# Kernel tuning notes

Hardware: AMD Instinct MI355X
Metric: run time of the kernel (lower is better)

## Reference

```python
import jax, jax.numpy as jnp
import numpy as np
from jax import lax

B, C, H, W = 8, 128, 64, 64
L = H * W  # 4096, multiple of 64 so BiMamba2's pad-to-chunk is a no-op
DM, DI, DS, DC, NH, HD = 32, 64, 64, 4, 1, 64  # d_model, d_inner, d_state, d_conv, nheads, headdim


def setup_inputs() -> dict:
    key = jax.random.key(0)
    ks = jax.random.split(key, 12)
    def r(i, shape, s):
        return jax.random.normal(ks[i], shape, jnp.float32) * s
    return {
        "x": jax.random.normal(ks[0], (B, C, H, W), jnp.float32),
        "lin1_w": r(1, (C, C), 0.05), "lin1_b": jnp.zeros((C,), jnp.float32),
        "dw_w": r(2, (C, 1, 3, 3), 0.1), "dw_b": jnp.zeros((C,), jnp.float32),
        "fc_in_w": r(3, (C, DM), 0.05),
        "mam_in_w": r(4, (2, DM, 2 * DI + 2 * DS + NH), 0.05),
        "mam_conv_w": r(5, (2, DI + 2 * DS, DC), 0.1),
        "mam_conv_b": jnp.zeros((2, DI + 2 * DS), jnp.float32),
        "mam_dt_bias": r(6, (2, NH), 0.1),
        "mam_A_log": jnp.zeros((2, NH), jnp.float32),
        "mam_D": jnp.ones((2, NH), jnp.float32),
        "mam_norm_w": jnp.ones((2, DI), jnp.float32),
        "mam_out_w": r(7, (2, DI, DM), 0.05),
        "fc_out_w": r(8, (DM, C), 0.05),
        "bn_g": jnp.ones((C,), jnp.float32), "bn_b": jnp.zeros((C,), jnp.float32),
        "conv4_w": r(9, (C, C), 0.05), "conv4_b": jnp.zeros((C,), jnp.float32),
    }


def _causal_dwconv1d(x, w, b):
    # x: (B, L, Ch); w: (Ch, DC) depthwise causal kernel (torch Conv1d groups=Ch, pad=DC-1, trimmed)
    xc = jnp.transpose(x, (0, 2, 1))
    xc = jnp.pad(xc, ((0, 0), (0, 0), (DC - 1, 0)))
    o = lax.conv_general_dilated(xc, w[:, None, :], (1,), "VALID",
                                 feature_group_count=w.shape[0],
                                 dimension_numbers=("NCH", "OIH", "NCH"))
    return jnp.transpose(o + b[None, :, None], (0, 2, 1))


def _mamba2(u, W_in, conv_w, conv_b, dt_bias, A_log, D, norm_w, W_out):
    # u: (B, L, DM). Minimal Mamba2 block: in_proj -> causal dwconv/silu -> selective scan -> gated RMSNorm -> out_proj
    b, l, _ = u.shape
    zxbcdt = u @ W_in                         # (b, l, 2*DI + 2*DS + NH)
    z = zxbcdt[..., :DI]
    xBC = zxbcdt[..., DI:DI + DI + 2 * DS]
    dt = zxbcdt[..., -NH:]
    xBC = jax.nn.silu(_causal_dwconv1d(xBC, conv_w, conv_b))
    xs = xBC[..., :DI]
    Bm = xBC[..., DI:DI + DS]                 # (b, l, DS)
    Cm = xBC[..., DI + DS:]                   # (b, l, DS)
    dt = jax.nn.softplus(dt + dt_bias)        # (b, l, NH)
    dA = jnp.exp(dt * (-jnp.exp(A_log)))      # (b, l, NH)
    xh = xs.reshape(b, l, NH, HD)
    dtx = dt[..., None] * xh                  # (b, l, NH, HD)

    def step(h, inp):
        dA_t, dtx_t, B_t, C_t = inp
        h = dA_t[:, :, None, None] * h + dtx_t[..., None] * B_t[:, None, None, :]
        y = jnp.einsum("bhpn,bn->bhp", h, C_t)
        return h, y

    h0 = jnp.zeros((b, NH, HD, DS), u.dtype)
    _, ys = lax.scan(step, h0, (jnp.moveaxis(dA, 1, 0), jnp.moveaxis(dtx, 1, 0),
                                jnp.moveaxis(Bm, 1, 0), jnp.moveaxis(Cm, 1, 0)))
    y = jnp.moveaxis(ys, 0, 1) + D[None, None, :, None] * xh   # (b, l, NH, HD)
    y = y.reshape(b, l, DI)
    y = y * jax.nn.silu(z)                    # gated RMSNorm
    y = y * lax.rsqrt(jnp.mean(y * y, -1, keepdims=True) + 1e-5) * norm_w
    return y @ W_out                          # (b, l, DM)


def _forward(x, lin1_w, lin1_b, dw_w, dw_b, fc_in_w, mam_in_w, mam_conv_w, mam_conv_b,
             mam_dt_bias, mam_A_log, mam_D, mam_norm_w, mam_out_w, fc_out_w,
             bn_g, bn_b, conv4_w, conv4_b):
    b, c, h, w = x.shape
    o = jnp.einsum("bihw,io->bohw", x, lin1_w) + lin1_b[None, :, None, None]
    o = lax.conv_general_dilated(o, dw_w, (1, 1), "SAME", feature_group_count=c,
                                 dimension_numbers=("NCHW", "OIHW", "NCHW")) + dw_b[None, :, None, None]
    o = jax.nn.silu(o)
    # BiMamba2_2D: flatten HxW -> sequence, fc_in, forward + reversed Mamba2, fc_out
    s = jnp.einsum("bcl,cd->bld", o.reshape(b, c, h * w), fc_in_w)
    y1 = _mamba2(s, mam_in_w[0], mam_conv_w[0], mam_conv_b[0], mam_dt_bias[0],
                 mam_A_log[0], mam_D[0], mam_norm_w[0], mam_out_w[0])
    y2 = jnp.flip(_mamba2(jnp.flip(s, 1), mam_in_w[1], mam_conv_w[1], mam_conv_b[1],
                          mam_dt_bias[1], mam_A_log[1], mam_D[1], mam_norm_w[1], mam_out_w[1]), 1)
    o = jnp.transpose((y1 + y2) @ fc_out_w, (0, 2, 1)).reshape(b, c, h, w)
    # BatchNorm2d (training-mode batch statistics)
    mu = jnp.mean(o, (0, 2, 3), keepdims=True)
    var = jnp.mean((o - mu) ** 2, (0, 2, 3), keepdims=True)
    o = (o - mu) * lax.rsqrt(var + 1e-5) * bn_g[None, :, None, None] + bn_b[None, :, None, None]
    g = jax.nn.sigmoid(jnp.einsum("bihw,io->bohw", o, conv4_w) + conv4_b[None, :, None, None])
    return g * x + x


def reference(x, lin1_w, lin1_b, dw_w, dw_b, fc_in_w, mam_in_w, mam_conv_w, mam_conv_b,
              mam_dt_bias, mam_A_log, mam_D, mam_norm_w, mam_out_w, fc_out_w,
              bn_g, bn_b, conv4_w, conv4_b):
    return _forward(x, lin1_w, lin1_b, dw_w, dw_b, fc_in_w, mam_in_w, mam_conv_w, mam_conv_b,
                    mam_dt_bias, mam_A_log, mam_D, mam_norm_w, mam_out_w, fc_out_w,
                    bn_g, bn_b, conv4_w, conv4_b)
```

## Files before the change

kernel.cpp:

```cpp
#include <hip/hip_runtime.h>
#include <math.h>

constexpr int Bn = 8, Cn = 128, Ln = 4096;

constexpr size_t OFF_O1   = 0;
constexpr size_t OFF_O2   = 4194304;
constexpr size_t OFF_S    = 8388608;
constexpr size_t OFF_Z    = 9437184;
constexpr size_t OFF_WT   = 11534336;
constexpr size_t OFF_XBCA = 13631488;
constexpr size_t OFF_DTS  = 26214400;
constexpr size_t OFF_CUM  = 26279936;
constexpr size_t OFF_T    = 26345472;
constexpr size_t OFF_SPREV= 30539776;
constexpr size_t OFF_S2A  = 34734080;
constexpr size_t OFF_S2B  = 35782656;
constexpr size_t OFF_BN   = 36831232;
constexpr size_t OFF_XX   = 36831488;
constexpr size_t OFF_WB1  = 38928640;
constexpr size_t OFF_WB4  = 38936832;
constexpr size_t OFF_WN   = 38945024;
constexpr size_t OFF_O3   = 0;

constexpr long XSTRIDE_H = 6291456;
constexpr long TSTRIDE = 2097152;

typedef __attribute__((ext_vector_type(8))) short short8;
typedef __attribute__((ext_vector_type(4))) float f32x4;
typedef __attribute__((ext_vector_type(4))) unsigned short us4;
typedef __attribute__((ext_vector_type(8))) unsigned short us8;

__device__ __forceinline__ float siluf(float v) { return v / (1.0f + expf(-v)); }

__device__ __forceinline__ unsigned short tobf(float f) {
  unsigned int u = __float_as_uint(f);
  u += 0x7FFFu + ((u >> 16) & 1u);
  return (unsigned short)(u >> 16);
}

__device__ __forceinline__ float frombf(unsigned short u) {
  return __uint_as_float(((unsigned int)u) << 16);
}

__device__ __forceinline__ unsigned int pk2(float a, float b) {
  return (unsigned int)tobf(a) | ((unsigned int)tobf(b) << 16);
}

__device__ __forceinline__ short8 ldfrag(const unsigned short* p) {
  union { unsigned int u[4]; short8 s; } cv;
  cv.u[0] = *(const unsigned int*)(p);
  cv.u[1] = *(const unsigned int*)(p + 2);
  cv.u[2] = *(const unsigned int*)(p + 4);
  cv.u[3] = *(const unsigned int*)(p + 6);
  return cv.s;
}

__global__ void k_prepc(const float* __restrict__ lin1_w, const float* __restrict__ conv4_w,
                        const float* __restrict__ normw, const float* __restrict__ Wout,
                        unsigned short* __restrict__ wb1, unsigned short* __restrict__ wb4,
                        unsigned short* __restrict__ wn) {
  int blk = blockIdx.x, tid = threadIdx.x;
  if (blk < 2) {
    const float* src = blk ? conv4_w : lin1_w;
    unsigned short* dst = blk ? wb4 : wb1;
    for (int idx = tid * 4; idx < 16384; idx += 1024) {
      float4 v = *(const float4*)&src[idx];
      us4 o;
      o[0] = tobf(v.x); o[1] = tobf(v.y); o[2] = tobf(v.z); o[3] = tobf(v.w);
      *(us4*)&dst[idx] = o;
    }
  } else {
    int dir = blk - 2;
    for (int idx = tid; idx < 2048; idx += 256) {
      int d = idx >> 6, p = idx & 63;
      wn[dir * 2048 + idx] = tobf(normw[dir * 64 + p] * Wout[(long)dir * 2048 + p * 32 + d]);
    }
  }
}

__global__ __launch_bounds__(256) void k_lin1(const float* __restrict__ x,
                                              const unsigned short* __restrict__ wb,
                                              const float* __restrict__ bias,
                                              unsigned short* __restrict__ o1) {
  __shared__ unsigned short wT[64][140];
  __shared__ unsigned short xT[64][140];
  int b = blockIdx.y, l0 = blockIdx.x * 64, cb = blockIdx.z * 64;
  int tid = threadIdx.x, lane = tid & 63, mt = tid >> 6;
  int q = lane >> 4, i = lane & 15;
  int c4 = (tid & 15) * 4, k0 = (tid >> 4) * 2;
#pragma unroll
  for (int s = 0; s < 4; ++s) {
    int k = k0 + s * 32;
    us4 w0 = *(const us4*)&wb[k * 128 + cb + c4];
    us4 w1 = *(const us4*)&wb[(k + 1) * 128 + cb + c4];
#pragma unroll
    for (int j = 0; j < 4; ++j)
      *(unsigned int*)&wT[c4 + j][k] =
          (unsigned int)w0[j] | ((unsigned int)w1[j] << 16);
    float4 x0 = *(const float4*)&x[((long)b * 128 + k) * 4096 + l0 + c4];
    float4 x1 = *(const float4*)&x[((long)b * 128 + k + 1) * 4096 + l0 + c4];
    *(unsigned int*)&xT[c4 + 0][k] = pk2(x0.x, x1.x);
    *(unsigned int*)&xT[c4 + 1][k] = pk2(x0.y, x1.y);
    *(unsigned int*)&xT[c4 + 2][k] = pk2(x0.z, x1.z);
    *(unsigned int*)&xT[c4 + 3][k] = pk2(x0.w, x1.w);
  }
  __syncthreads();
  short8 af[4];
#pragma unroll
  for (int kk = 0; kk < 4; ++kk)
    af[kk] = ldfrag(&wT[mt * 16 + i][q * 8 + 32 * kk]);
  float bv[4];
#pragma unroll
  for (int r2 = 0; r2 < 4; ++r2) bv[r2] = bias[cb + 16 * mt + q * 4 + r2];
#pragma unroll
  for (int nt = 0; nt < 4; ++nt) {
    f32x4 d = {0.f, 0.f, 0.f, 0.f};
#pragma unroll
    for (int kk = 0; kk < 4; ++kk) {
      short8 bfr = ldfrag(&xT[nt * 16 + i][q * 8 + 32 * kk]);
      d = __builtin_amdgcn_mfma_f32_16x16x32_bf16(af[kk], bfr, d, 0, 0, 0);
    }
#pragma unroll
    for (int r2 = 0; r2 < 4; ++r2) {
      int c = 16 * mt + q * 4 + r2;
      o1[((long)b * 128 + cb + c) * 4096 + l0 + nt * 16 + i] = tobf(d[r2] + bv[r2]);
    }
  }
}

__global__ void k_dw(const unsigned short* __restrict__ o1,
                     const float* __restrict__ wgt,
                     const float* __restrict__ bias, unsigned short* __restrict__ o2) {
  __shared__ float p[4096];
  int bc = blockIdx.x, c = bc & 127, tid = threadIdx.x;
  const unsigned short* src = o1 + (long)bc * 4096;
#pragma unroll
  for (int s4 = 0; s4 < 2; ++s4) {
    int off = s4 * 2048 + tid * 8;
    us8 v = *(const us8*)&src[off];
#pragma unroll
    for (int j = 0; j < 8; ++j) p[off + j] = frombf(v[j]);
  }
  float wr[9];
#pragma unroll
  for (int j = 0; j < 9; ++j) wr[j] = wgt[c * 9 + j];
  float bv = bias[c];
  __syncthreads();
  int wg = tid & 15, hs = tid >> 4;
  int w0 = wg * 4, h0 = hs * 4;
  float in[6][6];
#pragma unroll
  for (int ri = 0; ri < 6; ++ri) {
    int h = h0 - 1 + ri;
    if (h < 0 || h > 63) {
#pragma unroll
      for (int ci = 0; ci < 6; ++ci) in[ri][ci] = 0.f;
    } else {
      float4 cc = *(float4*)&p[h * 64 + w0];
      in[ri][1] = cc.x; in[ri][2] = cc.y; in[ri][3] = cc.z; in[ri][4] = cc.w;
      in[ri][0] = (w0 > 0) ? p[h * 64 + w0 - 1] : 0.f;
      in[ri][5] = (w0 < 60) ? p[h * 64 + w0 + 4] : 0.f;
    }
  }
#pragma unroll
  for (int r = 0; r < 4; ++r) {
    us4 oc;
#pragma unroll
    for (int q = 0; q < 4; ++q) {
      float acc = bv;
#pragma unroll
      for (int dh = 0; dh < 3; ++dh)
#pragma unroll
        for (int dq = 0; dq < 3; ++dq)
          acc += in[r + dh][q + dq] * wr[dh * 3 + dq];
      oc[q] = tobf(siluf(acc));
    }
    *(us4*)&o2[(long)bc * 4096 + (h0 + r) * 64 + w0] = oc;
  }
}

__global__ void k_fcin(const unsigned short* __restrict__ o2, const float* __restrict__ w,
                       unsigned short* __restrict__ sb,
                       const float* __restrict__ Win, unsigned short* __restrict__ WT) {
  __shared__ float xt[128][64];
  __shared__ float wt[128][32];
  int b = blockIdx.y, l0 = blockIdx.x * 64;
  int tid = threadIdx.x;
  int f4 = (tid & 15) * 4, r0 = tid >> 4;
#pragma unroll
  for (int st = 0; st < 8; ++st) {
    int r = r0 + st * 16;
    us4 v = *(const us4*)&o2[((long)b * 128 + r) * 4096 + l0 + f4];
#pragma unroll
    for (int j = 0; j < 4; ++j) xt[r][f4 + j] = frombf(v[j]);
  }
  int f4w = (tid & 7) * 4, rw = tid >> 3;
#pragma unroll
  for (int st = 0; st < 4; ++st) {
    int r = rw + st * 32;
    *(float4*)&wt[r][f4w] = *(const float4*)&w[r * 32 + f4w];
  }
  __syncthreads();
  int tx = tid & 15, ty = tid >> 4;
  int c0 = tx * 4, d0 = ty * 2;
  float acc[2][4] = {};
  for (int k = 0; k < 128; ++k) {
    float4 xv = *(float4*)&xt[k][c0];
    float2 wv = *(float2*)&wt[k][d0];
    float xa[4] = {xv.x, xv.y, xv.z, xv.w};
#pragma unroll
    for (int q = 0; q < 4; ++q) {
      acc[0][q] += wv.x * xa[q];
      acc[1][q] += wv.y * xa[q];
    }
  }
#pragma unroll
  for (int q = 0; q < 4; ++q) {
    long ob = ((long)b * 4096 + l0 + c0 + q) * 32 + d0;
    *(unsigned int*)&sb[ob] = pk2(acc[0][q], acc[1][q]);
  }
  if (blockIdx.y == 0 && blockIdx.x < 2) {
    int dir = blockIdx.x;
    for (int idx = tid; idx < 272 * 32; idx += 256) {
      int n = idx >> 5, kk = idx & 31;
      float v = (n < 257) ? Win[dir * 32 * 257 + kk * 257 + n] : 0.f;
      WT[dir * 8704 + idx] = tobf(v);
    }
  }
}

__global__ __launch_bounds__(256) void k_inprojconv(
    const unsigned short* __restrict__ sb, const unsigned short* __restrict__ WT,
    const float* __restrict__ conv_w, const float* __restrict__ conv_b,
    const float* __restrict__ dt_bias, const float* __restrict__ A_log,
    unsigned short* __restrict__ zT, unsigned short* __restrict__ xbca,
    unsigned short* __restrict__ xX,
    float* __restrict__ dts, float* __restrict__ cum,
    unsigned short* __restrict__ Tg) {
  __shared__ unsigned short xbcT[192][82];
  __shared__ float dtL[64];
  __shared__ float dtsS[64], cumSS[64], fL[64];
  int dir = blockIdx.z, b = blockIdx.y, l0 = blockIdx.x * 64;
  int tid = threadIdx.x, lane = tid & 63, mt = tid >> 6;
  int q = lane >> 4, i = lane & 15;
  long rowbase = (long)b * 4096 + l0;
  const unsigned short* W = WT + (long)dir * 8704;
  const short8 zfrag = {0, 0, 0, 0, 0, 0, 0, 0};

  if (mt == 0) {
    short8 afr[4];
#pragma unroll
    for (int rt = 0; rt < 4; ++rt) {
      int l = l0 + 16 * rt + i;
      int lsrc = dir ? (4095 - l) : l;
      afr[rt] = *(const short8*)&sb[((long)b * 4096 + lsrc) * 32 + q * 8];
    }
#pragma unroll
    for (int ct = 0; ct < 4; ++ct) {
      int n = 16 * ct + i;
      short8 bfr = *(const short8*)&W[n * 32 + q * 8];
      unsigned short* zrow = zT + (((long)dir * 64 + n) * 8 + b) * 4096 + l0 + q * 4;
#pragma unroll
      for (int rt = 0; rt < 4; ++rt) {
        f32x4 d = {0.f, 0.f, 0.f, 0.f};
        d = __builtin_amdgcn_mfma_f32_16x16x32_bf16(afr[rt], bfr, d, 0, 0, 0);
        us4 pk;
        pk[0] = tobf(d[0]); pk[1] = tobf(d[1]);
        pk[2] = tobf(d[2]); pk[3] = tobf(d[3]);
        *(us4*)&zrow[16 * rt] = pk;
      }
    }
    {
      short8 bfr = *(const short8*)&W[(256 + i) * 32 + q * 8];
#pragma unroll
      for (int rt = 0; rt < 4; ++rt) {
        f32x4 d = {0.f, 0.f, 0.f, 0.f};
        d = __builtin_amdgcn_mfma_f32_16x16x32_bf16(afr[rt], bfr, d, 0, 0, 0);
        if (i == 0) {
#pragma unroll
          for (int r2 = 0; r2 < 4; ++r2) dtL[16 * rt + q * 4 + r2] = d[r2];
        }
      }
    }
  } else {
    short8 afr[5];
#pragma unroll
    for (int rt = 0; rt < 5; ++rt) {
      int l = l0 - 3 + 16 * rt + i;
      if (l >= 0 && l < 4096) {
        int lsrc = dir ? (4095 - l) : l;
        afr[rt] = *(const short8*)&sb[((long)b * 4096 + lsrc) * 32 + q * 8];
      } else {
        afr[rt] = zfrag;
      }
    }
#pragma unroll
    for (int cti = 0; cti < 4; ++cti) {
      int n = 16 * (mt * 4 + cti) + i;
      short8 bfr = *(const short8*)&W[n * 32 + q * 8];
      int cc = n - 64;
#pragma unroll
      for (int rt = 0; rt < 5; ++rt) {
        f32x4 d = {0.f, 0.f, 0.f, 0.f};
        d = __builtin_amdgcn_mfma_f32_16x16x32_bf16(afr[rt], bfr, d, 0, 0, 0);
        int rr0 = 16 * rt + q * 4;
        unsigned int p0 = (unsigned int)tobf(d[0]) | ((unsigned int)tobf(d[1]) << 16);
        unsigned int p1 = (unsigned int)tobf(d[2]) | ((unsigned int)tobf(d[3]) << 16);
        *(unsigned int*)&xbcT[cc][rr0] = p0;
        *(unsigned int*)&xbcT[cc][rr0 + 2] = p1;
      }
    }
  }
  __syncthreads();

  if (tid < 192) {
    int c = tid;
    float cw0 = conv_w[dir * 768 + c * 4 + 0];
    float cw1 = conv_w[dir * 768 + c * 4 + 1];
    float cw2 = conv_w[dir * 768 + c * 4 + 2];
    float cw3 = conv_w[dir * 768 + c * 4 + 3];
    float cb2 = conv_b[dir * 192 + c];
    unsigned short* xp = xbca + (long)dir * XSTRIDE_H;
    float win0 = 0.f, win1 = 0.f, win2 = 0.f, win3 = 0.f;
    for (int rp = 0; rp < 34; ++rp) {
      unsigned int pk = *(const unsigned int*)&xbcT[c][rp * 2];
      float a0 = frombf((unsigned short)(pk & 0xFFFFu));
      float a1 = frombf((unsigned short)(pk >> 16));
      int rr = rp * 2;
      win0 = win1; win1 = win2; win2 = win3; win3 = a0;
      if (rr >= 3 && rr <= 66) {
        float acc = cb2 + win0 * cw0 + win1 * cw1 + win2 * cw2 + win3 * cw3;
        float sv = siluf(acc);
        int t = rr - 3;
        if (c >= 64) xp[(rowbase + t) * 192 + c] = tobf(sv);
        if (c < 128) xbcT[c][t] = tobf(sv);
      }
      win0 = win1; win1 = win2; win2 = win3; win3 = a1;
      if (rr + 1 >= 3 && rr + 1 <= 66) {
        float acc = cb2 + win0 * cw0 + win1 * cw1 + win2 * cw2 + win3 * cw3;
        float sv = siluf(acc);
        int t = rr - 2;
        if (c >= 64) xp[(rowbase + t) * 192 + c] = tobf(sv);
        if (c < 128) xbcT[c][t] = tobf(sv);
      }
    }
  } else {
    int ln = tid - 192;
    float v = dtL[ln] + dt_bias[dir];
    float sp = (v > 20.f) ? v : log1pf(expf(v));
    dts[dir * 32768 + rowbase + ln] = sp;
    dtsS[ln] = sp;
    float cd = -expf(A_log[dir]) * sp;
#pragma unroll
    for (int off = 1; off < 64; off <<= 1) {
      float u = __shfl_up(cd, off);
      if (ln >= off) cd += u;
    }
    cum[dir * 32768 + rowbase + ln] = cd;
    cumSS[ln] = cd;
  }
  __syncthreads();

  {
    int r = tid >> 2, seg = (tid & 3) * 16;
    unsigned short* dst =
        xX + (((long)dir * 512 + b * 64 + blockIdx.x) * 64 + r) * 64 + seg;
#pragma unroll
    for (int j = 0; j < 8; ++j) {
      unsigned int v = *(const unsigned int*)&xbcT[r][seg + 2 * j];
      *(unsigned int*)(dst + 2 * j) = v;
    }
  }
  if (tid < 64) fL[tid] = expf(cumSS[63] - cumSS[tid]) * dtsS[tid];
  __syncthreads();

  {
    int c = tid & 63, tb2 = (tid >> 6) * 16;
#pragma unroll
    for (int j = 0; j < 8; ++j) {
      int t = tb2 + 2 * j;
      unsigned int pk = *(const unsigned int*)&xbcT[c][t];
      float v0 = frombf((unsigned short)(pk & 0xFFFFu));
      float v1 = frombf((unsigned short)(pk >> 16));
      unsigned int po = (unsigned int)tobf(v0 * fL[t]) |
                        ((unsigned int)tobf(v1 * fL[t + 1]) << 16);
      *(unsigned int*)&xbcT[c][t] = po;
    }
  }
  __syncthreads();

  {
    short8 a0 = ldfrag(&xbcT[mt * 16 + i][q * 8]);
    short8 a1 = ldfrag(&xbcT[mt * 16 + i][q * 8 + 32]);
    unsigned short* Tp = Tg + (long)dir * TSTRIDE + ((long)(b * 64 + blockIdx.x)) * 4096;
#pragma unroll
    for (int nt = 0; nt < 4; ++nt) {
      short8 b0 = ldfrag(&xbcT[64 + nt * 16 + i][q * 8]);
      short8 b1 = ldfrag(&xbcT[64 + nt * 16 + i][q * 8 + 32]);
      f32x4 d = {0.f, 0.f, 0.f, 0.f};
      d = __builtin_amdgcn_mfma_f32_16x16x32_bf16(a0, b0, d, 0, 0, 0);
      d = __builtin_amdgcn_mfma_f32_16x16x32_bf16(a1, b1, d, 0, 0, 0);
#pragma unroll
      for (int r2 = 0; r2 < 4; ++r2)
        Tp[(mt * 16 + q * 4 + r2) * 64 + nt * 16 + i] = tobf(d[r2]);
    }
  }
}

__global__ void k_scan(const unsigned short* __restrict__ T, const float* __restrict__ cum,
                       unsigned short* __restrict__ Sprev) {
  __shared__ float E[64];
  int blk = blockIdx.x;
  int dirb = blk >> 4;
  int dir = dirb >> 3, b = dirb & 7;
  int pn = (blk & 15) * 256 + threadIdx.x;
  const float* cp = cum + dir * 32768 + b * 4096;
  if (threadIdx.x < 64) E[threadIdx.x] = expf(cp[threadIdx.x * 64 + 63]);
  __syncthreads();
  const unsigned short* Tp = T + (long)dir * TSTRIDE + (long)b * 262144 + pn;
  unsigned short* Sp = Sprev + (long)dir * TSTRIDE + (long)b * 262144 + pn;
  float s0 = 0.f;
  float tb[16];
#pragma unroll
  for (int j = 0; j < 16; ++j) tb[j] = frombf(Tp[(long)j * 4096]);
  for (int kc = 0; kc < 4; ++kc) {
    float tn[16];
    if (kc < 3) {
#pragma unroll
      for (int j = 0; j < 16; ++j)
        tn[j] = frombf(Tp[(long)(kc * 16 + 16 + j) * 4096]);
    }
#pragma unroll
    for (int j = 0; j < 16; ++j) {
      int k = kc * 16 + j;
      Sp[(long)k * 4096] = tobf(s0);
      s0 = fmaf(E[k], s0, tb[j]);
    }
    if (kc < 3) {
#pragma unroll
      for (int j = 0; j < 16; ++j) tb[j] = tn[j];
    }
  }
}

__global__ __launch_bounds__(256) void k_chunkYout(
    const unsigned short* __restrict__ xbca, const float* __restrict__ dts,
    const float* __restrict__ cum, const unsigned short* __restrict__ Sprev,
    const float* __restrict__ Dp, const unsigned short* __restrict__ zT,
    const unsigned short* __restrict__ xX, const unsigned short* __restrict__ wn,
    unsigned short* __restrict__ s2a, unsigned short* __restrict__ s2b) {
  __shared__ unsigned short Gb[64][72];
  __shared__ float cumS[64], dtS[64];
  int dir = blockIdx.y;
  int bk = blockIdx.x, b = bk >> 6, k = bk & 63;
  int tid = threadIdx.x, lane = tid & 63, mt = tid >> 6;
  int q = lane >> 4, i = lane & 15;
  const unsigned short* xp = xbca + (long)dir * XSTRIDE_H;
  const float* dtp = dts + dir * 32768;
  const float* cp = cum + dir * 32768;
  const unsigned short* Sp = Sprev + (long)dir * TSTRIDE;
  const unsigned short* xXp = xX + ((long)dir * 512 + bk) * 4096;
  const unsigned short* wnp = wn + dir * 2048;
  long base = (long)b * 4096 + (long)k * 64;

  if (tid < 64) { cumS[tid] = cp[base + tid]; dtS[tid] = dtp[base + tid]; }
  __syncthreads();

  const unsigned short* crow = &xp[(base + mt * 16 + i) * 192];
  short8 a0 = *(const short8*)&crow[128 + q * 8];
  short8 a1 = *(const short8*)&crow[160 + q * 8];

  f32x4 dint[4];
#pragma unroll
  for (int lt = 0; lt < 4; ++lt) {
    const unsigned short* sp8 = &Sp[(long)bk * 4096 + (lt * 16 + i) * 64 + q * 8];
    short8 b0 = *(const short8*)sp8;
    short8 b1 = *(const short8*)(sp8 + 32);
    f32x4 d = {0.f, 0.f, 0.f, 0.f};
    d = __builtin_amdgcn_mfma_f32_16x16x32_bf16(a0, b0, d, 0, 0, 0);
    d = __builtin_amdgcn_mfma_f32_16x16x32_bf16(a1, b1, d, 0, 0, 0);
    dint[lt] = d;
  }

#pragma unroll
  for (int lt = 0; lt < 4; ++lt) {
    int r = lt * 16 + i;
    float dtv = dtS[r];
    const unsigned short* brow = &xp[(base + r) * 192 + 64];
    us8 bv0 = *(const us8*)&brow[q * 8];
    us8 bv1 = *(const us8*)&brow[32 + q * 8];
    union { unsigned short us[8]; short8 s8; } c0, c1;
#pragma unroll
    for (int j = 0; j < 8; ++j) {
      c0.us[j] = tobf(frombf(bv0[j]) * dtv);
      c1.us[j] = tobf(frombf(bv1[j]) * dtv);
    }
    f32x4 d = {0.f, 0.f, 0.f, 0.f};
    d = __builtin_amdgcn_mfma_f32_16x16x32_bf16(a0, c0.s8, d, 0, 0, 0);
    d = __builtin_amdgcn_mfma_f32_16x16x32_bf16(a1, c1.s8, d, 0, 0, 0);
#pragma unroll
    for (int r2 = 0; r2 < 4; ++r2) {
      int t = mt * 16 + q * 4 + r2;
      int l = lt * 16 + i;
      float g = (l <= t) ? d[r2] * expf(cumS[t] - cumS[l]) : 0.f;
      Gb[t][l] = tobf(g);
    }
  }

  short8 g0 = *(const short8*)&Gb[mt * 16 + i][q * 8];
  short8 g1 = *(const short8*)&Gb[mt * 16 + i][q * 8 + 32];
  float Dv = Dp[dir];
  float et4[4];
#pragma unroll
  for (int r2 = 0; r2 < 4; ++r2) et4[r2] = expf(cumS[mt * 16 + q * 4 + r2]);
  float yv[4][4];
  float rowss[4] = {0.f, 0.f, 0.f, 0.f};
#pragma unroll
  for (int lt = 0; lt < 4; ++lt) {
    const unsigned short* xrow = &xXp[(lt * 16 + i) * 64];
    short8 b0 = *(const short8*)&xrow[q * 8];
    short8 b1 = *(const short8*)&xrow[q * 8 + 32];
    f32x4 d = {0.f, 0.f, 0.f, 0.f};
    d = __builtin_amdgcn_mfma_f32_16x16x32_bf16(g0, b0, d, 0, 0, 0);
    d = __builtin_amdgcn_mfma_f32_16x16x32_bf16(g1, b1, d, 0, 0, 0);
    us4 zq = *(const us4*)&zT[(((long)dir * 64 + lt * 16 + i) * 8 + b) * 4096 +
                              (long)k * 64 + mt * 16 + q * 4];
    unsigned int xpk0 = *(const unsigned int*)&xrow[mt * 16 + q * 4];
    unsigned int xpk1 = *(const unsigned int*)&xrow[mt * 16 + q * 4 + 2];
    float xvr[4];
    xvr[0] = frombf((unsigned short)(xpk0 & 0xFFFFu));
    xvr[1] = frombf((unsigned short)(xpk0 >> 16));
    xvr[2] = frombf((unsigned short)(xpk1 & 0xFFFFu));
    xvr[3] = frombf((unsigned short)(xpk1 >> 16));
#pragma unroll
    for (int r2 = 0; r2 < 4; ++r2) {
      float y = d[r2] + et4[r2] * dint[lt][r2] + Dv * xvr[r2];
      float zv = frombf(zq[r2]);
      float v = y * siluf(zv);
      yv[lt][r2] = v;
      rowss[r2] += v * v;
    }
  }
#pragma unroll
  for (int m = 1; m < 16; m <<= 1) {
#pragma unroll
    for (int r2 = 0; r2 < 4; ++r2) rowss[r2] += __shfl_xor(rowss[r2], m);
  }
  float rscv[4];
#pragma unroll
  for (int r2 = 0; r2 < 4; ++r2)
    rscv[r2] = rsqrtf(rowss[r2] * (1.0f / 64.0f) + 1e-5f);
#pragma unroll
  for (int lt = 0; lt < 4; ++lt)
#pragma unroll
    for (int r2 = 0; r2 < 4; ++r2) {
      int t = mt * 16 + q * 4 + r2;
      int p = lt * 16 + i;
      Gb[t][p] = tobf(yv[lt][r2] * rscv[r2]);
    }

  short8 y0 = *(const short8*)&Gb[mt * 16 + i][q * 8];
  short8 y1 = *(const short8*)&Gb[mt * 16 + i][q * 8 + 32];
  unsigned short* s2x = dir ? s2b : s2a;
#pragma unroll
  for (int dt = 0; dt < 2; ++dt) {
    const unsigned short* wrow = &wnp[(dt * 16 + i) * 64];
    short8 b0 = *(const short8*)&wrow[q * 8];
    short8 b1 = *(const short8*)&wrow[q * 8 + 32];
    f32x4 d = {0.f, 0.f, 0.f, 0.f};
    d = __builtin_amdgcn_mfma_f32_16x16x32_bf16(y0, b0, d, 0, 0, 0);
    d = __builtin_amdgcn_mfma_f32_16x16x32_bf16(y1, b1, d, 0, 0, 0);
#pragma unroll
    for (int r2 = 0; r2 < 4; ++r2) {
      int tl = mt * 16 + q * 4 + r2;
      int l = k * 64 + tl;
      int lout = dir ? (4095 - l) : l;
      int dd = dt * 16 + i;
      s2x[((long)b * 4096 + lout) * 32 + dd] = tobf(d[r2]);
    }
  }
}

__global__ void k_fcout(const unsigned short* __restrict__ s2a,
                        const unsigned short* __restrict__ s2b,
                        const float* __restrict__ w, unsigned short* __restrict__ o3,
                        float* __restrict__ part) {
  __shared__ float st[32][68];
  __shared__ float wt[32][64];
  int b = blockIdx.y, l0 = blockIdx.x * 64, cb = blockIdx.z * 64;
  int tid = threadIdx.x;
  {
    int d = tid & 31, l = tid >> 5;
    for (int si = 0; si < 8; ++si) {
      int ll = l + si * 8;
      long o = ((long)b * 4096 + l0 + ll) * 32 + d;
      st[d][ll] = frombf(s2a[o]) + frombf(s2b[o]);
    }
    int f4 = (tid & 15) * 4, r = tid >> 4;
    for (int si = 0; si < 2; ++si) {
      int rr = r + si * 16;
      *(float4*)&wt[rr][f4] = *(const float4*)&w[rr * 128 + cb + f4];
    }
  }
  __syncthreads();
  int tx = tid & 15, ty = tid >> 4;
  int c0 = tx * 4, t0 = ty * 4;
  float acc[4][4] = {};
  for (int k = 0; k < 32; ++k) {
    float4 xv = *(float4*)&st[k][c0];
    float4 wv = *(float4*)&wt[k][t0];
    float xa[4] = {xv.x, xv.y, xv.z, xv.w};
    float wa[4] = {wv.x, wv.y, wv.z, wv.w};
#pragma unroll
    for (int a = 0; a < 4; ++a)
#pragma unroll
      for (int q = 0; q < 4; ++q) acc[a][q] += wa[a] * xa[q];
  }
#pragma unroll
  for (int a = 0; a < 4; ++a) {
    us4 pk;
#pragma unroll
    for (int q = 0; q < 4; ++q) pk[q] = tobf(acc[a][q]);
    *(us4*)&o3[((long)b * 128 + cb + t0 + a) * 4096 + l0 + c0] = pk;
  }
  float ssum[4], sqq[4];
#pragma unroll
  for (int a = 0; a < 4; ++a) {
    ssum[a] = acc[a][0] + acc[a][1] + acc[a][2] + acc[a][3];
    sqq[a] = acc[a][0] * acc[a][0] + acc[a][1] * acc[a][1] +
             acc[a][2] * acc[a][2] + acc[a][3] * acc[a][3];
  }
#pragma unroll
  for (int m = 1; m < 16; m <<= 1) {
#pragma unroll
    for (int a = 0; a < 4; ++a) {
      ssum[a] += __shfl_xor(ssum[a], m);
      sqq[a] += __shfl_xor(sqq[a], m);
    }
  }
  if (tx == 0) {
    int idx = b * 64 + blockIdx.x;
#pragma unroll
    for (int a = 0; a < 4; ++a) {
      int ch = cb + t0 + a;
      part[(long)ch * 512 + idx] = ssum[a];
      part[65536 + (long)ch * 512 + idx] = sqq[a];
    }
  }
}

__global__ void k_bnred(const float* __restrict__ part, float* __restrict__ stats) {
  int ch = blockIdx.x, tid = threadIdx.x;
  float s = part[(long)ch * 512 + tid] + part[(long)ch * 512 + 256 + tid];
  float q = part[65536 + (long)ch * 512 + tid] +
            part[65536 + (long)ch * 512 + 256 + tid];
  for (int off = 32; off; off >>= 1) {
    s += __shfl_down(s, off);
    q += __shfl_down(q, off);
  }
  __shared__ float rs[4], rq[4];
  if ((tid & 63) == 0) { rs[tid >> 6] = s; rq[tid >> 6] = q; }
  __syncthreads();
  if (tid == 0) {
    stats[ch] = rs[0] + rs[1] + rs[2] + rs[3];
    stats[128 + ch] = rq[0] + rq[1] + rq[2] + rq[3];
  }
}

__global__ __launch_bounds__(256) void k_final(const unsigned short* __restrict__ o3,
                                               const float* __restrict__ stats,
                                               const float* __restrict__ bng,
                                               const float* __restrict__ bnb,
                                               const unsigned short* __restrict__ wb,
                                               const float* __restrict__ bias,
                                               const float* __restrict__ x,
                                               float* __restrict__ out) {
  __shared__ unsigned short wT[64][140];
  __shared__ unsigned short aT[64][140];
  __shared__ float sc[128], sh[128];
  int b = blockIdx.y, l0 = blockIdx.x * 64, cb = blockIdx.z * 64;
  int tid = threadIdx.x, lane = tid & 63, mt = tid >> 6;
  int q = lane >> 4, i = lane & 15;
  if (tid < 128) {
    float mu = stats[tid] * (1.0f / 32768.0f);
    float var = stats[128 + tid] * (1.0f / 32768.0f) - mu * mu;
    float r = rsqrtf(var + 1e-5f);
    sc[tid] = r * bng[tid];
    sh[tid] = bnb[tid] - mu * r * bng[tid];
  }
  __syncthreads();
  int c4 = (tid & 15) * 4, k0 = (tid >> 4) * 2;
#pragma unroll
  for (int s = 0; s < 4; ++s) {
    int k = k0 + s * 32;
    us4 w0 = *(const us4*)&wb[k * 128 + cb + c4];
    us4 w1 = *(const us4*)&wb[(k + 1) * 128 + cb + c4];
#pragma unroll
    for (int j = 0; j < 4; ++j)
      *(unsigned int*)&wT[c4 + j][k] =
          (unsigned int)w0[j] | ((unsigned int)w1[j] << 16);
    us4 a0 = *(const us4*)&o3[((long)b * 128 + k) * 4096 + l0 + c4];
    us4 a1 = *(const us4*)&o3[((long)b * 128 + k + 1) * 4096 + l0 + c4];
    float sc0 = sc[k], sh0 = sh[k], sc1 = sc[k + 1], sh1 = sh[k + 1];
#pragma unroll
    for (int j = 0; j < 4; ++j) {
      *(unsigned int*)&aT[c4 + j][k] =
          pk2(fmaf(frombf(a0[j]), sc0, sh0), fmaf(frombf(a1[j]), sc1, sh1));
    }
  }
  __syncthreads();
  short8 af[4];
#pragma unroll
  for (int kk = 0; kk < 4; ++kk)
    af[kk] = ldfrag(&wT[mt * 16 + i][q * 8 + 32 * kk]);
  float bv[4];
#pragma unroll
  for (int r2 = 0; r2 < 4; ++r2) bv[r2] = bias[cb + 16 * mt + q * 4 + r2];
#pragma unroll
  for (int nt = 0; nt < 4; ++nt) {
    f32x4 d = {0.f, 0.f, 0.f, 0.f};
#pragma unroll
    for (int kk = 0; kk < 4; ++kk) {
      short8 bfr = ldfrag(&aT[nt * 16 + i][q * 8 + 32 * kk]);
      d = __builtin_amdgcn_mfma_f32_16x16x32_bf16(af[kk], bfr, d, 0, 0, 0);
    }
#pragma unroll
    for (int r2 = 0; r2 < 4; ++r2) {
      int c = 16 * mt + q * 4 + r2;
      long xi = ((long)b * 128 + cb + c) * 4096 + l0 + nt * 16 + i;
      float g = 1.0f / (1.0f + expf(-(d[r2] + bv[r2])));
      out[xi] = x[xi] * (1.0f + g);
    }
  }
}

extern "C" void kernel_launch(void* const* d_in, const int* in_sizes, int n_in,
                              void* d_out, int out_size, void* d_ws, size_t ws_size,
                              hipStream_t stream) {
  const float* x          = (const float*)d_in[0];
  const float* lin1_w     = (const float*)d_in[1];
  const float* lin1_b     = (const float*)d_in[2];
  const float* dw_w       = (const float*)d_in[3];
  const float* dw_b       = (const float*)d_in[4];
  const float* fc_in_w    = (const float*)d_in[5];
  const float* mam_in_w   = (const float*)d_in[6];
  const float* mam_conv_w = (const float*)d_in[7];
  const float* mam_conv_b = (const float*)d_in[8];
  const float* mam_dt_bias= (const float*)d_in[9];
  const float* mam_A_log  = (const float*)d_in[10];
  const float* mam_D      = (const float*)d_in[11];
  const float* mam_norm_w = (const float*)d_in[12];
  const float* mam_out_w  = (const float*)d_in[13];
  const float* fc_out_w   = (const float*)d_in[14];
  const float* bn_g       = (const float*)d_in[15];
  const float* bn_b       = (const float*)d_in[16];
  const float* conv4_w    = (const float*)d_in[17];
  const float* conv4_b    = (const float*)d_in[18];
  float* out = (float*)d_out;
  float* ws  = (float*)d_ws;

  unsigned short* o1h  = (unsigned short*)(ws + OFF_O1);
  unsigned short* o2h  = (unsigned short*)(ws + OFF_O2);
  unsigned short* sbuf = (unsigned short*)(ws + OFF_S);
  unsigned short* zTb  = (unsigned short*)(ws + OFF_Z);
  unsigned short* WTb  = (unsigned short*)(ws + OFF_WT);
  unsigned short* xbca = (unsigned short*)(ws + OFF_XBCA);
  float* dts  = ws + OFF_DTS;
  float* cum  = ws + OFF_CUM;
  unsigned short* Tbufh = (unsigned short*)(ws + OFF_T);
  unsigned short* Sprev = (unsigned short*)(ws + OFF_SPREV);
  unsigned short* s2a = (unsigned short*)(ws + OFF_S2A);
  unsigned short* s2b = (unsigned short*)(ws + OFF_S2B);
  float* bnst = ws + OFF_BN;
  unsigned short* xXb = (unsigned short*)(ws + OFF_XX);
  unsigned short* wb1 = (unsigned short*)(ws + OFF_WB1);
  unsigned short* wb4 = (unsigned short*)(ws + OFF_WB4);
  unsigned short* wnb = (unsigned short*)(ws + OFF_WN);
  unsigned short* o3h = (unsigned short*)(ws + OFF_O3);
  float* part = ws + OFF_T;

  k_prepc<<<4, 256, 0, stream>>>(lin1_w, conv4_w, mam_norm_w, mam_out_w, wb1, wb4, wnb);
  k_lin1<<<dim3(64, 8, 2), 256, 0, stream>>>(x, wb1, lin1_b, o1h);
  k_dw<<<1024, 256, 0, stream>>>(o1h, dw_w, dw_b, o2h);
  k_fcin<<<dim3(64, 8), 256, 0, stream>>>(o2h, fc_in_w, sbuf, mam_in_w, WTb);
  k_inprojconv<<<dim3(64, 8, 2), 256, 0, stream>>>(sbuf, WTb, mam_conv_w, mam_conv_b,
                                                   mam_dt_bias, mam_A_log,
                                                   zTb, xbca, xXb, dts, cum, Tbufh);
  k_scan<<<256, 256, 0, stream>>>(Tbufh, cum, Sprev);
  k_chunkYout<<<dim3(512, 2), 256, 0, stream>>>(xbca, dts, cum, Sprev, mam_D, zTb,
                                                xXb, wnb, s2a, s2b);
  k_fcout<<<dim3(64, 8, 2), 256, 0, stream>>>(s2a, s2b, fc_out_w, o3h, part);
  k_bnred<<<128, 256, 0, stream>>>(part, bnst);
  k_final<<<dim3(64, 8, 2), 256, 0, stream>>>(o3h, bnst, bn_g, bn_b, wb4, conv4_b, x, out);
}
```

Measured before the change: 206.4 us.

## Fuse depthwise 3x3 conv with fc_in projection into one row-tiled kernel

Merges the depthwise conv+SiLU kernel and the fc_in projection into a single kernel that processes one image row per block. Each block stages three halo rows for all channels in shared memory, computes the conv, and then does the 128->32 projection from shared memory. This removes the bf16 intermediate o2 write and read and one launch. The Win transpose also moves into the prep kernel. The trade-off is that each input row is loaded three times across blocks because of the halo, and the block uses more shared memory.

Result: slower. 225.4 us (+9.2%).

```diff
diff --git a/kernel.cpp b/kernel.cpp
--- a/kernel.cpp
+++ b/kernel.cpp
@@ -57,8 +57,9 @@
 
 __global__ void k_prepc(const float* __restrict__ lin1_w, const float* __restrict__ conv4_w,
                         const float* __restrict__ normw, const float* __restrict__ Wout,
+                        const float* __restrict__ Win,
                         unsigned short* __restrict__ wb1, unsigned short* __restrict__ wb4,
-                        unsigned short* __restrict__ wn) {
+                        unsigned short* __restrict__ wn, unsigned short* __restrict__ WT) {
   int blk = blockIdx.x, tid = threadIdx.x;
   if (blk < 2) {
     const float* src = blk ? conv4_w : lin1_w;
@@ -69,11 +70,18 @@
       o[0] = tobf(v.x); o[1] = tobf(v.y); o[2] = tobf(v.z); o[3] = tobf(v.w);
       *(us4*)&dst[idx] = o;
     }
-  } else {
+  } else if (blk < 4) {
     int dir = blk - 2;
     for (int idx = tid; idx < 2048; idx += 256) {
       int d = idx >> 6, p = idx & 63;
       wn[dir * 2048 + idx] = tobf(normw[dir * 64 + p] * Wout[(long)dir * 2048 + p * 32 + d]);
+    }
+  } else {
+    int dir = blk - 4;
+    for (int idx = tid; idx < 272 * 32; idx += 256) {
+      int n = idx >> 5, kk = idx & 31;
+      float v = (n < 257) ? Win[dir * 32 * 257 + kk * 257 + n] : 0.f;
+      WT[dir * 8704 + idx] = tobf(v);
     }
   }
 }
@@ -128,105 +136,83 @@
   }
 }
 
-__global__ void k_dw(const unsigned short* __restrict__ o1,
-                     const float* __restrict__ wgt,
-                     const float* __restrict__ bias, unsigned short* __restrict__ o2) {
-  __shared__ float p[4096];
-  int bc = blockIdx.x, c = bc & 127, tid = threadIdx.x;
-  const unsigned short* src = o1 + (long)bc * 4096;
-#pragma unroll
-  for (int s4 = 0; s4 < 2; ++s4) {
-    int off = s4 * 2048 + tid * 8;
-    us8 v = *(const us8*)&src[off];
-#pragma unroll
-    for (int j = 0; j < 8; ++j) p[off + j] = frombf(v[j]);
-  }
-  float wr[9];
-#pragma unroll
-  for (int j = 0; j < 9; ++j) wr[j] = wgt[c * 9 + j];
-  float bv = bias[c];
-  __syncthreads();
-  int wg = tid & 15, hs = tid >> 4;
-  int w0 = wg * 4, h0 = hs * 4;
-  float in[6][6];
-#pragma unroll
-  for (int ri = 0; ri < 6; ++ri) {
-    int h = h0 - 1 + ri;
-    if (h < 0 || h > 63) {
-#pragma unroll
-      for (int ci = 0; ci < 6; ++ci) in[ri][ci] = 0.f;
+__global__ __launch_bounds__(256) void k_dwfc(
+    const unsigned short* __restrict__ o1, const float* __restrict__ wgt,
+    const float* __restrict__ bias, const float* __restrict__ fcw,
+    unsigned short* __restrict__ sb) {
+  __shared__ unsigned short pin[3][128][64];
+  __shared__ float fw[128][32];
+  int h = blockIdx.x, b = blockIdx.y, tid = threadIdx.x;
+
+  for (int u = tid; u < 3072; u += 256) {
+    int off = u * 8;
+    int hr = off >> 13, rem = off & 8191;
+    int c = rem >> 6, w = rem & 63;
+    int hh = h - 1 + hr;
+    us8 v;
+    if (hh >= 0 && hh < 64) {
+      v = *(const us8*)&o1[((long)b * 128 + c) * 4096 + hh * 64 + w];
     } else {
-      float4 cc = *(float4*)&p[h * 64 + w0];
-      in[ri][1] = cc.x; in[ri][2] = cc.y; in[ri][3] = cc.z; in[ri][4] = cc.w;
-      in[ri][0] = (w0 > 0) ? p[h * 64 + w0 - 1] : 0.f;
-      in[ri][5] = (w0 < 60) ? p[h * 64 + w0 + 4] : 0.f;
-    }
-  }
-#pragma unroll
-  for (int r = 0; r < 4; ++r) {
-    us4 oc;
-#pragma unroll
-    for (int q = 0; q < 4; ++q) {
+#pragma unroll
+      for (int j = 0; j < 8; ++j) v[j] = 0;
+    }
+    *(us8*)&pin[hr][c][w] = v;
+  }
+  for (int u = tid * 4; u < 4096; u += 1024) {
+    int c = u >> 5, d = u & 31;
+    *(float4*)&fw[c][d] = *(const float4*)&fcw[c * 32 + d];
+  }
+  __syncthreads();
+
+  int w0 = (tid & 31) * 2, c0 = (tid >> 5) * 16;
+  float ocv[16][2];
+#pragma unroll
+  for (int ci = 0; ci < 16; ++ci) {
+    int c = c0 + ci;
+    float wr[9];
+#pragma unroll
+    for (int j = 0; j < 9; ++j) wr[j] = wgt[c * 9 + j];
+    float bv = bias[c];
+    float rv[3][4];
+#pragma unroll
+    for (int dh = 0; dh < 3; ++dh)
+#pragma unroll
+      for (int j = 0; j < 4; ++j) {
+        int ww = w0 - 1 + j;
+        rv[dh][j] = (ww >= 0 && ww < 64) ? frombf(pin[dh][c][ww]) : 0.f;
+      }
+#pragma unroll
+    for (int wi = 0; wi < 2; ++wi) {
       float acc = bv;
 #pragma unroll
       for (int dh = 0; dh < 3; ++dh)
 #pragma unroll
-        for (int dq = 0; dq < 3; ++dq)
-          acc += in[r + dh][q + dq] * wr[dh * 3 + dq];
-      oc[q] = tobf(siluf(acc));
-    }
-    *(us4*)&o2[(long)bc * 4096 + (h0 + r) * 64 + w0] = oc;
-  }
-}
-
-__global__ void k_fcin(const unsigned short* __restrict__ o2, const float* __restrict__ w,
-                       unsigned short* __restrict__ sb,
-                       const float* __restrict__ Win, unsigned short* __restrict__ WT) {
-  __shared__ float xt[128][64];
-  __shared__ float wt[128][32];
-  int b = blockIdx.y, l0 = blockIdx.x * 64;
-  int tid = threadIdx.x;
-  int f4 = (tid & 15) * 4, r0 = tid >> 4;
-#pragma unroll
-  for (int st = 0; st < 8; ++st) {
-    int r = r0 + st * 16;
-    us4 v = *(const us4*)&o2[((long)b * 128 + r) * 4096 + l0 + f4];
-#pragma unroll
-    for (int j = 0; j < 4; ++j) xt[r][f4 + j] = frombf(v[j]);
-  }
-  int f4w = (tid & 7) * 4, rw = tid >> 3;
-#pragma unroll
-  for (int st = 0; st < 4; ++st) {
-    int r = rw + st * 32;
-    *(float4*)&wt[r][f4w] = *(const float4*)&w[r * 32 + f4w];
-  }
-  __syncthreads();
-  int tx = tid & 15, ty = tid >> 4;
-  int c0 = tx * 4, d0 = ty * 2;
-  float acc[2][4] = {};
-  for (int k = 0; k < 128; ++k) {
-    float4 xv = *(float4*)&xt[k][c0];
-    float2 wv = *(float2*)&wt[k][d0];
-    float xa[4] = {xv.x, xv.y, xv.z, xv.w};
-#pragma unroll
-    for (int q = 0; q < 4; ++q) {
-      acc[0][q] += wv.x * xa[q];
-      acc[1][q] += wv.y * xa[q];
-    }
-  }
-#pragma unroll
-  for (int q = 0; q < 4; ++q) {
-    long ob = ((long)b * 4096 + l0 + c0 + q) * 32 + d0;
-    *(unsigned int*)&sb[ob] = pk2(acc[0][q], acc[1][q]);
-  }
-  if (blockIdx.y == 0 && blockIdx.x < 2) {
-    int dir = blockIdx.x;
-    for (int idx = tid; idx < 272 * 32; idx += 256) {
-      int n = idx >> 5, kk = idx & 31;
-      float v = (n < 257) ? Win[dir * 32 * 257 + kk * 257 + n] : 0.f;
-      WT[dir * 8704 + idx] = tobf(v);
-    }
-  }
+        for (int dw = 0; dw < 3; ++dw)
+          acc += rv[dh][wi + dw] * wr[dh * 3 + dw];
+      ocv[ci][wi] = siluf(acc);
+    }
+  }
+  __syncthreads();
+#pragma unroll
+  for (int ci = 0; ci < 16; ++ci)
+    *(unsigned int*)&pin[0][c0 + ci][w0] = pk2(ocv[ci][0], ocv[ci][1]);
+  __syncthreads();
+
+  int w = tid & 63, d0 = (tid >> 6) * 8;
+  float acc[8] = {};
+  for (int c = 0; c < 128; ++c) {
+    float a = frombf(pin[0][c][w]);
+    float4 f0 = *(const float4*)&fw[c][d0];
+    float4 f1 = *(const float4*)&fw[c][d0 + 4];
+    acc[0] += a * f0.x; acc[1] += a * f0.y;
+    acc[2] += a * f0.z; acc[3] += a * f0.w;
+    acc[4] += a * f1.x; acc[5] += a * f1.y;
+    acc[6] += a * f1.z; acc[7] += a * f1.w;
+  }
+  long ob = ((long)b * 4096 + h * 64 + w) * 32 + d0;
+#pragma unroll
+  for (int j = 0; j < 4; ++j)
+    *(unsigned int*)&sb[ob + 2 * j] = pk2(acc[2 * j], acc[2 * j + 1]);
 }
 
 __global__ __launch_bounds__(256) void k_inprojconv(
@@ -760,7 +746,6 @@
   float* ws  = (float*)d_ws;
 
   unsigned short* o1h  = (unsigned short*)(ws + OFF_O1);
-  unsigned short* o2h  = (unsigned short*)(ws + OFF_O2);
   unsigned short* sbuf = (unsigned short*)(ws + OFF_S);
   unsigned short* zTb  = (unsigned short*)(ws + OFF_Z);
   unsigned short* WTb  = (unsigned short*)(ws + OFF_WT);
@@ -779,10 +764,10 @@
   unsigned short* o3h = (unsigned short*)(ws + OFF_O3);
   float* part = ws + OFF_T;
 
-  k_prepc<<<4, 256, 0, stream>>>(lin1_w, conv4_w, mam_norm_w, mam_out_w, wb1, wb4, wnb);
+  k_prepc<<<6, 256, 0, stream>>>(lin1_w, conv4_w, mam_norm_w, mam_out_w, mam_in_w,
+                                 wb1, wb4, wnb, WTb);
   k_lin1<<<dim3(64, 8, 2), 256, 0, stream>>>(x, wb1, lin1_b, o1h);
-  k_dw<<<1024, 256, 0, stream>>>(o1h, dw_w, dw_b, o2h);
-  k_fcin<<<dim3(64, 8), 256, 0, stream>>>(o2h, fc_in_w, sbuf, mam_in_w, WTb);
+  k_dwfc<<<dim3(64, 8), 256, 0, stream>>>(o1h, dw_w, dw_b, fc_in_w, sbuf);
   k_inprojconv<<<dim3(64, 8, 2), 256, 0, stream>>>(sbuf, WTb, mam_conv_w, mam_conv_b,
                                                    mam_dt_bias, mam_A_log,
                                                    zTb, xbca, xXb, dts, cum, Tbufh);
```
